# Kernel optimization log

Hardware: AMD Instinct MI355X
Metric: run time of the kernel (lower is better)

## Reference

```python
import jax, jax.numpy as jnp
import numpy as np

B, C_CLS, D_WORD, J = 1024, 80, 300, 8000
IMG_CH = 2048

def setup_inputs() -> dict:
    key = jax.random.key(0)
    ks = jax.random.split(key, 9)
    return {
        'feature': jax.random.normal(ks[0], (B, IMG_CH), jnp.float32),
        'inp': jax.random.normal(ks[1], (1, C_CLS, D_WORD), jnp.float32),
        'A': jax.random.uniform(ks[2], (C_CLS, C_CLS), jnp.float32),
        'W_gc1': jax.random.normal(ks[3], (D_WORD, 1024), jnp.float32) * (1.0 / np.sqrt(1024)),
        'W_gc2': jax.random.normal(ks[4], (1024, 2048), jnp.float32) * (1.0 / np.sqrt(2048)),
        'W_img': jax.random.normal(ks[5], (J, IMG_CH), jnp.float32) * 0.02,
        'b_img': jax.random.normal(ks[6], (J,), jnp.float32) * 0.02,
        'W_cls': jax.random.normal(ks[7], (J, 2048), jnp.float32) * 0.02,
        'b_cls': jax.random.normal(ks[8], (J,), jnp.float32) * 0.02,
    }

def _gen_adj(A):
    # torch: D = A.sum(1)**-0.5; adj = (A @ diag(D)).T @ diag(D) = D[:,None]*A.T*D[None,:]
    D = jnp.power(jnp.sum(A, axis=1), -0.5)
    return D[:, None] * A.T * D[None, :]

def reference(feature, inp, A, W_gc1, W_gc2, W_img, b_img, W_cls, b_cls):
    inp0 = inp[0]                                   # [C, 300]
    adj = jax.lax.stop_gradient(_gen_adj(A))        # [C, C], .detach() in torch
    x = adj @ (inp0 @ W_gc1)                        # gc1: [C, 1024]
    x = jax.nn.leaky_relu(x, negative_slope=0.2)
    x = adj @ (x @ W_gc2)                           # gc2: [C, 2048]
    # MFB bilinear pooling (is_usemfb=True, is_hash=False -> out_in_tmp=1, eval-mode dropout=identity)
    # original: out[b,c] = sum_j (Linear_img(feature[b])[j] * Linear_cls(x_col_c)[j])
    img_proj = feature @ W_img.T + b_img            # [B, J]
    cls_proj = x @ W_cls.T + b_cls                  # [C, J]
    x_out = img_proj @ cls_proj.T                   # [B, C]
    return x_out
```

## Files before the change

### kernel.cpp

```cpp
#include <hip/hip_runtime.h>
#include <hip/hip_bf16.h>


typedef __bf16 bf16_t;
typedef __bf16 bf16x8 __attribute__((ext_vector_type(8)));
typedef float f32x4 __attribute__((ext_vector_type(4)));

#define MFMA16(a, b, c) __builtin_amdgcn_mfma_f32_16x16x32_bf16((a), (b), (c), 0, 0, 0)

__device__ inline bf16x8 cvt8(float4 a, float4 b) {
  bf16x8 v;
  v[0] = (bf16_t)a.x; v[1] = (bf16_t)a.y; v[2] = (bf16_t)a.z; v[3] = (bf16_t)a.w;
  v[4] = (bf16_t)b.x; v[5] = (bf16_t)b.y; v[6] = (bf16_t)b.z; v[7] = (bf16_t)b.w;
  return v;
}

__global__ void k_adj(const float* __restrict__ A, float* __restrict__ adj) {
  __shared__ float Dv[80];
  int tid = threadIdx.x;
  if (tid < 80) {
    float s = 0.f;
    #pragma unroll 4
    for (int j = 0; j < 80; ++j) s += A[tid * 80 + j];
    Dv[tid] = rsqrtf(s);
  }
  __syncthreads();
  for (int idx = tid; idx < 6400; idx += blockDim.x) {
    int i = idx / 80, j = idx % 80;
    adj[idx] = Dv[i] * Dv[j] * A[j * 80 + i];
  }
}

__global__ void k_cvt0(const float* __restrict__ inp0, bf16_t* __restrict__ x0b) {
  int idx = blockIdx.x * blockDim.x + threadIdx.x;
  if (idx < 30720) {
    int c = idx / 384, k = idx % 384;
    x0b[idx] = (k < 300) ? (bf16_t)inp0[c * 300 + k] : (bf16_t)0.f;
  }
}

__global__ __launch_bounds__(256) void k_gc1m(
    const bf16_t* __restrict__ x0b, const float* __restrict__ Wgc1,
    float* __restrict__ t1) {
  int tid = threadIdx.x;
  int w = tid >> 6, l = tid & 63;
  int ln = l & 15, q = l >> 4;
  int n0 = blockIdx.x * 16;

  __shared__ float red[4][80][16];
  f32x4 acc[5] = {};
  for (int ks = 0; ks < 3; ++ks) {
    int kq = w * 96 + ks * 32 + q * 8;
    bf16x8 bfrag;
    #pragma unroll
    for (int jj = 0; jj < 8; ++jj) {
      int k = kq + jj;
      int kc = k < 300 ? k : 299;
      float wv = Wgc1[kc * 1024 + n0 + ln];
      bfrag[jj] = (bf16_t)(k < 300 ? wv : 0.f);
    }
    #pragma unroll
    for (int mt = 0; mt < 5; ++mt) {
      bf16x8 afrag = *(const bf16x8*)(x0b + (size_t)(mt * 16 + ln) * 384 + kq);
      acc[mt] = MFMA16(afrag, bfrag, acc[mt]);
    }
  }
  #pragma unroll
  for (int mt = 0; mt < 5; ++mt)
    #pragma unroll
    for (int reg = 0; reg < 4; ++reg)
      red[w][mt * 16 + q * 4 + reg][ln] = acc[mt][reg];
  __syncthreads();
  for (int o = tid; o < 1280; o += 256) {
    int c = o >> 4, nn = o & 15;
    t1[c * 1024 + n0 + nn] = red[0][c][nn] + red[1][c][nn] + red[2][c][nn] + red[3][c][nn];
  }
}

__global__ void k_adjmul_leaky(const float* __restrict__ adj, const float* __restrict__ t1,
                               bf16_t* __restrict__ x1b) {
  int idx = blockIdx.x * blockDim.x + threadIdx.x;
  int c = idx >> 10, n = idx & 1023;
  const float* ar = adj + c * 80;
  float acc = 0.f;
  #pragma unroll 4
  for (int cc = 0; cc < 80; ++cc) acc += ar[cc] * t1[cc * 1024 + n];
  x1b[idx] = (bf16_t)(acc > 0.f ? acc : 0.2f * acc);
}

__global__ __launch_bounds__(256) void k_gc2m(
    const bf16_t* __restrict__ x1b, const float* __restrict__ Wgc2,
    float* __restrict__ t2) {
  int tid = threadIdx.x;
  int w = tid >> 6, l = tid & 63;
  int ln = l & 15, q = l >> 4;
  int nc = blockIdx.x & 31, kc = blockIdx.x >> 5;

  __shared__ float Bs[32][66];
  f32x4 acc[5] = {};
  for (int s = 0; s < 2; ++s) {
    int k0 = kc * 64 + s * 32;
    #pragma unroll
    for (int it = 0; it < 2; ++it) {
      int slot = tid + it * 256;
      int kr = slot >> 4, nq = slot & 15;
      const float4 v = *(const float4*)(Wgc2 + (size_t)(k0 + kr) * 2048 + nc * 64 + nq * 4);
      *(float4*)&Bs[kr][nq * 4] = v;
    }
    __syncthreads();
    bf16x8 bfrag;
    #pragma unroll
    for (int jj = 0; jj < 8; ++jj) bfrag[jj] = (bf16_t)Bs[q * 8 + jj][w * 16 + ln];
    #pragma unroll
    for (int mt = 0; mt < 5; ++mt) {
      bf16x8 afrag = *(const bf16x8*)(x1b + (size_t)(mt * 16 + ln) * 1024 + k0 + q * 8);
      acc[mt] = MFMA16(afrag, bfrag, acc[mt]);
    }
    __syncthreads();
  }
  #pragma unroll
  for (int mt = 0; mt < 5; ++mt)
    #pragma unroll
    for (int reg = 0; reg < 4; ++reg)
      atomicAdd(&t2[(size_t)(mt * 16 + q * 4 + reg) * 2048 + nc * 64 + w * 16 + ln],
                acc[mt][reg]);
}

__global__ void k_adjmul_bf16(const float* __restrict__ adj, const float* __restrict__ t2,
                              bf16_t* __restrict__ x2) {
  int idx = blockIdx.x * blockDim.x + threadIdx.x;
  int c = idx >> 11, n = idx & 2047;
  const float* ar = adj + c * 80;
  float acc = 0.f;
  #pragma unroll 4
  for (int cc = 0; cc < 80; ++cc) acc += ar[cc] * t2[cc * 2048 + n];
  x2[idx] = (bf16_t)acc;
}

__global__ __launch_bounds__(512) void k_clsproj(
    const float* __restrict__ Wcls, const float* __restrict__ bcls,
    const float* __restrict__ bimg, const bf16_t* __restrict__ x2,
    bf16_t* __restrict__ P, float* __restrict__ r) {
  int tid = threadIdx.x;
  int w = tid >> 6, l = tid & 63;
  int ln = l & 15, q = l >> 4;
  int j0 = blockIdx.x * 16;
  size_t jrow = (size_t)(j0 + ln) * 2048;

  __shared__ float red[8][80][16];
  __shared__ float rloc[80];
  if (tid < 80) rloc[tid] = 0.f;

  f32x4 acc[5] = {};
  int kbase = w * 256 + q * 8;
  for (int ks = 0; ks < 8; ++ks) {
    int kq = kbase + ks * 32;
    const float4* bp = (const float4*)(Wcls + jrow + kq);
    float4 b0 = bp[0], b1 = bp[1];
    bf16x8 bfrag = cvt8(b0, b1);
    #pragma unroll
    for (int mt = 0; mt < 5; ++mt) {
      bf16x8 afrag = *(const bf16x8*)(x2 + (size_t)(mt * 16 + ln) * 2048 + kq);
      acc[mt] = MFMA16(afrag, bfrag, acc[mt]);
    }
  }
  #pragma unroll
  for (int mt = 0; mt < 5; ++mt)
    #pragma unroll
    for (int reg = 0; reg < 4; ++reg)
      red[w][mt * 16 + q * 4 + reg][ln] = acc[mt][reg];
  __syncthreads();

  for (int o = tid; o < 1280; o += 512) {
    int c = o >> 4, jj = o & 15;
    float v = bcls[j0 + jj];
    #pragma unroll
    for (int ww = 0; ww < 8; ++ww) v += red[ww][c][jj];
    P[(size_t)c * 8000 + j0 + jj] = (bf16_t)v;
    atomicAdd(&rloc[c], bimg[j0 + jj] * v);
  }
  __syncthreads();
  if (tid < 80) atomicAdd(&r[tid], rloc[tid]);
}

__global__ __launch_bounds__(256) void k_hmat(
    const float* __restrict__ Wimg, const bf16_t* __restrict__ P, float* __restrict__ H) {
  int tid = threadIdx.x;
  int w = tid >> 6, l = tid & 63;
  int ln = l & 15, q = l >> 4;
  int nc = blockIdx.x & 31, jc = blockIdx.x >> 5;
  int jbase = jc * 160;

  __shared__ float Bs[160][66];
  float4 v[10];
  #pragma unroll
  for (int it = 0; it < 10; ++it) {
    int slot = tid + it * 256;
    int jr = slot >> 4, nq = slot & 15;
    v[it] = *(const float4*)(Wimg + (size_t)(jbase + jr) * 2048 + nc * 64 + nq * 4);
  }
  #pragma unroll
  for (int it = 0; it < 10; ++it) {
    int slot = tid + it * 256;
    int jr = slot >> 4, nq = slot & 15;
    *(float4*)&Bs[jr][nq * 4] = v[it];
  }
  __syncthreads();

  f32x4 acc[5] = {};
  for (int s = 0; s < 5; ++s) {
    bf16x8 bfrag;
    #pragma unroll
    for (int jj = 0; jj < 8; ++jj) bfrag[jj] = (bf16_t)Bs[s * 32 + q * 8 + jj][w * 16 + ln];
    #pragma unroll
    for (int mt = 0; mt < 5; ++mt) {
      bf16x8 afrag =
          *(const bf16x8*)(P + (size_t)(mt * 16 + ln) * 8000 + jbase + s * 32 + q * 8);
      acc[mt] = MFMA16(afrag, bfrag, acc[mt]);
    }
  }
  #pragma unroll
  for (int mt = 0; mt < 5; ++mt)
    #pragma unroll
    for (int reg = 0; reg < 4; ++reg)
      atomicAdd(&H[(size_t)(mt * 16 + q * 4 + reg) * 2048 + nc * 64 + w * 16 + ln],
                acc[mt][reg]);
}

__global__ __launch_bounds__(256) void k_out(
    const float* __restrict__ feat, const float* __restrict__ H,
    const float* __restrict__ r, float* __restrict__ out) {
  int tid = threadIdx.x;
  int w = tid >> 6, l = tid & 63;
  int ln = l & 15, q = l >> 4;
  int mg = blockIdx.x & 15, kc = blockIdx.x >> 4;
  int m0 = mg * 64 + w * 16;
  size_t frow = (size_t)(m0 + ln) * 2048;

  f32x4 acc[5] = {};
  int kbase = kc * 256 + q * 8;
  for (int ks = 0; ks < 8; ++ks) {
    int kq = kbase + ks * 32;
    const float4* ap = (const float4*)(feat + frow + kq);
    bf16x8 afrag = cvt8(ap[0], ap[1]);
    #pragma unroll
    for (int nt = 0; nt < 5; ++nt) {
      const float4* hp = (const float4*)(H + (size_t)(nt * 16 + ln) * 2048 + kq);
      bf16x8 bfrag = cvt8(hp[0], hp[1]);
      acc[nt] = MFMA16(afrag, bfrag, acc[nt]);
    }
  }
  #pragma unroll
  for (int nt = 0; nt < 5; ++nt)
    #pragma unroll
    for (int reg = 0; reg < 4; ++reg) {
      int b = m0 + q * 4 + reg;
      int c = nt * 16 + ln;
      float v = acc[nt][reg];
      if (kc == 0) v += r[c];
      atomicAdd(&out[b * 80 + c], v);
    }
}

extern "C" void kernel_launch(void* const* d_in, const int* in_sizes, int n_in,
                              void* d_out, int out_size, void* d_ws, size_t ws_size,
                              hipStream_t stream) {
  const float* feature = (const float*)d_in[0];
  const float* inp     = (const float*)d_in[1];
  const float* A       = (const float*)d_in[2];
  const float* Wgc1    = (const float*)d_in[3];
  const float* Wgc2    = (const float*)d_in[4];
  const float* Wimg    = (const float*)d_in[5];
  const float* bimg    = (const float*)d_in[6];
  const float* Wcls    = (const float*)d_in[7];
  const float* bcls    = (const float*)d_in[8];
  float* out = (float*)d_out;

  char* ws = (char*)d_ws;
  float*  adj = (float*)(ws + 0);
  float*  t1  = (float*)(ws + 25600);
  bf16_t* x1b = (bf16_t*)(ws + 353280);
  float*  t2  = (float*)(ws + 517120);
  bf16_t* x2  = (bf16_t*)(ws + 1172480);
  bf16_t* P   = (bf16_t*)(ws + 1500160);
  float*  H   = (float*)(ws + 2780160);
  float*  r   = (float*)(ws + 3435520);
  bf16_t* x0b = (bf16_t*)(ws + 3435840);

  hipMemsetAsync(t2, 0, 80 * 2048 * 4, stream);
  hipMemsetAsync(H, 0, 80 * 2048 * 4, stream);
  hipMemsetAsync(r, 0, 80 * 4, stream);
  hipMemsetAsync(out, 0, 1024 * 80 * 4, stream);

  k_adj<<<1, 128, 0, stream>>>(A, adj);
  k_cvt0<<<120, 256, 0, stream>>>(inp, x0b);
  k_gc1m<<<64, 256, 0, stream>>>(x0b, Wgc1, t1);
  k_adjmul_leaky<<<320, 256, 0, stream>>>(adj, t1, x1b);
  k_gc2m<<<512, 256, 0, stream>>>(x1b, Wgc2, t2);
  k_adjmul_bf16<<<640, 256, 0, stream>>>(adj, t2, x2);
  k_clsproj<<<500, 512, 0, stream>>>(Wcls, bcls, bimg, x2, P, r);
  k_hmat<<<1600, 256, 0, stream>>>(Wimg, P, H);
  k_out<<<128, 256, 0, stream>>>(feature, H, r, out);
}
```

Measured before the change: 298.8 us.

## Replace atomic split-K accumulation with partial buffers and reduction kernels

The gc2 and H-matrix split-K kernels now write per-chunk partial sums to workspace buffers, and new reduction kernels (k_t2red, k_hred) sum them instead of using float atomicAdd. Each K chunk is doubled in size and staged through a double-buffered shared-memory tile with register prefetch of the next slice. k_out now reduces across K within a block through shared memory and writes the output directly. This removes most atomics and three memsets, at the cost of two extra launches and extra partial-buffer traffic (about 13 MB for Hp).

```diff
diff --git a/kernel.cpp b/kernel.cpp
--- a/kernel.cpp
+++ b/kernel.cpp
@@ -90,40 +90,59 @@
 
 __global__ __launch_bounds__(256) void k_gc2m(
     const bf16_t* __restrict__ x1b, const float* __restrict__ Wgc2,
-    float* __restrict__ t2) {
+    float* __restrict__ t2p) {
   int tid = threadIdx.x;
   int w = tid >> 6, l = tid & 63;
   int ln = l & 15, q = l >> 4;
   int nc = blockIdx.x & 31, kc = blockIdx.x >> 5;
-
-  __shared__ float Bs[32][66];
-  f32x4 acc[5] = {};
-  for (int s = 0; s < 2; ++s) {
-    int k0 = kc * 64 + s * 32;
+  const float* wbase = Wgc2 + (size_t)(kc * 128) * 2048 + nc * 64;
+
+  __shared__ float Bs[2][32][66];
+  float4 pv[2];
+  #pragma unroll
+  for (int it = 0; it < 2; ++it) {
+    int slot = tid + it * 256, kr = slot >> 4, nq = slot & 15;
+    pv[it] = *(const float4*)(wbase + (size_t)kr * 2048 + nq * 4);
+  }
+  f32x4 acc[5] = {};
+  for (int s = 0; s < 4; ++s) {
     #pragma unroll
     for (int it = 0; it < 2; ++it) {
-      int slot = tid + it * 256;
-      int kr = slot >> 4, nq = slot & 15;
-      const float4 v = *(const float4*)(Wgc2 + (size_t)(k0 + kr) * 2048 + nc * 64 + nq * 4);
-      *(float4*)&Bs[kr][nq * 4] = v;
+      int slot = tid + it * 256, kr = slot >> 4, nq = slot & 15;
+      *(float4*)&Bs[s & 1][kr][nq * 4] = pv[it];
     }
     __syncthreads();
+    if (s < 3) {
+      #pragma unroll
+      for (int it = 0; it < 2; ++it) {
+        int slot = tid + it * 256, kr = slot >> 4, nq = slot & 15;
+        pv[it] = *(const float4*)(wbase + (size_t)((s + 1) * 32 + kr) * 2048 + nq * 4);
+      }
+    }
+    int k0 = kc * 128 + s * 32;
     bf16x8 bfrag;
     #pragma unroll
-    for (int jj = 0; jj < 8; ++jj) bfrag[jj] = (bf16_t)Bs[q * 8 + jj][w * 16 + ln];
+    for (int jj = 0; jj < 8; ++jj) bfrag[jj] = (bf16_t)Bs[s & 1][q * 8 + jj][w * 16 + ln];
     #pragma unroll
     for (int mt = 0; mt < 5; ++mt) {
       bf16x8 afrag = *(const bf16x8*)(x1b + (size_t)(mt * 16 + ln) * 1024 + k0 + q * 8);
       acc[mt] = MFMA16(afrag, bfrag, acc[mt]);
     }
-    __syncthreads();
-  }
+  }
+  float* tp = t2p + (size_t)kc * 163840 + nc * 64 + w * 16 + ln;
   #pragma unroll
   for (int mt = 0; mt < 5; ++mt)
     #pragma unroll
     for (int reg = 0; reg < 4; ++reg)
-      atomicAdd(&t2[(size_t)(mt * 16 + q * 4 + reg) * 2048 + nc * 64 + w * 16 + ln],
-                acc[mt][reg]);
+      tp[(size_t)(mt * 16 + q * 4 + reg) * 2048] = acc[mt][reg];
+}
+
+__global__ void k_t2red(const float* __restrict__ t2p, float* __restrict__ t2) {
+  int i = blockIdx.x * 256 + threadIdx.x;
+  float s = 0.f;
+  #pragma unroll
+  for (int p = 0; p < 8; ++p) s += t2p[(size_t)p * 163840 + i];
+  t2[i] = s;
 }
 
 __global__ void k_adjmul_bf16(const float* __restrict__ adj, const float* __restrict__ t2,
@@ -184,61 +203,73 @@
 }
 
 __global__ __launch_bounds__(256) void k_hmat(
-    const float* __restrict__ Wimg, const bf16_t* __restrict__ P, float* __restrict__ H) {
+    const float* __restrict__ Wimg, const bf16_t* __restrict__ P, float* __restrict__ Hp) {
   int tid = threadIdx.x;
   int w = tid >> 6, l = tid & 63;
   int ln = l & 15, q = l >> 4;
   int nc = blockIdx.x & 31, jc = blockIdx.x >> 5;
-  int jbase = jc * 160;
-
-  __shared__ float Bs[160][66];
-  float4 v[10];
-  #pragma unroll
-  for (int it = 0; it < 10; ++it) {
-    int slot = tid + it * 256;
-    int jr = slot >> 4, nq = slot & 15;
-    v[it] = *(const float4*)(Wimg + (size_t)(jbase + jr) * 2048 + nc * 64 + nq * 4);
-  }
-  #pragma unroll
-  for (int it = 0; it < 10; ++it) {
-    int slot = tid + it * 256;
-    int jr = slot >> 4, nq = slot & 15;
-    *(float4*)&Bs[jr][nq * 4] = v[it];
-  }
-  __syncthreads();
-
-  f32x4 acc[5] = {};
-  for (int s = 0; s < 5; ++s) {
+  const float* wbase = Wimg + (size_t)(jc * 320) * 2048 + nc * 64;
+
+  __shared__ float Bs[2][32][66];
+  float4 pv[2];
+  #pragma unroll
+  for (int it = 0; it < 2; ++it) {
+    int slot = tid + it * 256, jr = slot >> 4, nq = slot & 15;
+    pv[it] = *(const float4*)(wbase + (size_t)jr * 2048 + nq * 4);
+  }
+  f32x4 acc[5] = {};
+  for (int s = 0; s < 10; ++s) {
+    #pragma unroll
+    for (int it = 0; it < 2; ++it) {
+      int slot = tid + it * 256, jr = slot >> 4, nq = slot & 15;
+      *(float4*)&Bs[s & 1][jr][nq * 4] = pv[it];
+    }
+    __syncthreads();
+    if (s < 9) {
+      #pragma unroll
+      for (int it = 0; it < 2; ++it) {
+        int slot = tid + it * 256, jr = slot >> 4, nq = slot & 15;
+        pv[it] = *(const float4*)(wbase + (size_t)((s + 1) * 32 + jr) * 2048 + nq * 4);
+      }
+    }
+    int j0 = jc * 320 + s * 32;
     bf16x8 bfrag;
     #pragma unroll
-    for (int jj = 0; jj < 8; ++jj) bfrag[jj] = (bf16_t)Bs[s * 32 + q * 8 + jj][w * 16 + ln];
+    for (int jj = 0; jj < 8; ++jj) bfrag[jj] = (bf16_t)Bs[s & 1][q * 8 + jj][w * 16 + ln];
     #pragma unroll
     for (int mt = 0; mt < 5; ++mt) {
-      bf16x8 afrag =
-          *(const bf16x8*)(P + (size_t)(mt * 16 + ln) * 8000 + jbase + s * 32 + q * 8);
+      bf16x8 afrag = *(const bf16x8*)(P + (size_t)(mt * 16 + ln) * 8000 + j0 + q * 8);
       acc[mt] = MFMA16(afrag, bfrag, acc[mt]);
     }
   }
+  float* hp = Hp + (size_t)jc * 163840 + nc * 64 + w * 16 + ln;
   #pragma unroll
   for (int mt = 0; mt < 5; ++mt)
     #pragma unroll
     for (int reg = 0; reg < 4; ++reg)
-      atomicAdd(&H[(size_t)(mt * 16 + q * 4 + reg) * 2048 + nc * 64 + w * 16 + ln],
-                acc[mt][reg]);
-}
-
-__global__ __launch_bounds__(256) void k_out(
+      hp[(size_t)(mt * 16 + q * 4 + reg) * 2048] = acc[mt][reg];
+}
+
+__global__ void k_hred(const float* __restrict__ Hp, float* __restrict__ H) {
+  int i = blockIdx.x * 256 + threadIdx.x;
+  float s = 0.f;
+  #pragma unroll
+  for (int p = 0; p < 25; ++p) s += Hp[(size_t)p * 163840 + i];
+  H[i] = s;
+}
+
+__global__ __launch_bounds__(512) void k_out(
     const float* __restrict__ feat, const float* __restrict__ H,
     const float* __restrict__ r, float* __restrict__ out) {
   int tid = threadIdx.x;
   int w = tid >> 6, l = tid & 63;
   int ln = l & 15, q = l >> 4;
-  int mg = blockIdx.x & 15, kc = blockIdx.x >> 4;
-  int m0 = mg * 64 + w * 16;
+  int m0 = blockIdx.x * 16;
   size_t frow = (size_t)(m0 + ln) * 2048;
 
-  f32x4 acc[5] = {};
-  int kbase = kc * 256 + q * 8;
+  __shared__ float red[8][16][80];
+  f32x4 acc[5] = {};
+  int kbase = w * 256 + q * 8;
   for (int ks = 0; ks < 8; ++ks) {
     int kq = kbase + ks * 32;
     const float4* ap = (const float4*)(feat + frow + kq);
@@ -253,13 +284,16 @@
   #pragma unroll
   for (int nt = 0; nt < 5; ++nt)
     #pragma unroll
-    for (int reg = 0; reg < 4; ++reg) {
-      int b = m0 + q * 4 + reg;
-      int c = nt * 16 + ln;
-      float v = acc[nt][reg];
-      if (kc == 0) v += r[c];
-      atomicAdd(&out[b * 80 + c], v);
-    }
+    for (int reg = 0; reg < 4; ++reg)
+      red[w][q * 4 + reg][nt * 16 + ln] = acc[nt][reg];
+  __syncthreads();
+  for (int o = tid; o < 1280; o += 512) {
+    int mm = o / 80, c = o % 80;
+    float v = r[c];
+    #pragma unroll
+    for (int ww = 0; ww < 8; ++ww) v += red[ww][mm][c];
+    out[(m0 + mm) * 80 + c] = v;
+  }
 }
 
 extern "C" void kernel_launch(void* const* d_in, const int* in_sizes, int n_in,
@@ -286,19 +320,20 @@
   float*  H   = (float*)(ws + 2780160);
   float*  r   = (float*)(ws + 3435520);
   bf16_t* x0b = (bf16_t*)(ws + 3435840);
-
-  hipMemsetAsync(t2, 0, 80 * 2048 * 4, stream);
-  hipMemsetAsync(H, 0, 80 * 2048 * 4, stream);
+  float*  t2p = (float*)(ws + 3497280);
+  float*  Hp  = (float*)(ws + 8740160);
+
   hipMemsetAsync(r, 0, 80 * 4, stream);
-  hipMemsetAsync(out, 0, 1024 * 80 * 4, stream);
 
   k_adj<<<1, 128, 0, stream>>>(A, adj);
   k_cvt0<<<120, 256, 0, stream>>>(inp, x0b);
   k_gc1m<<<64, 256, 0, stream>>>(x0b, Wgc1, t1);
   k_adjmul_leaky<<<320, 256, 0, stream>>>(adj, t1, x1b);
-  k_gc2m<<<512, 256, 0, stream>>>(x1b, Wgc2, t2);
+  k_gc2m<<<256, 256, 0, stream>>>(x1b, Wgc2, t2p);
+  k_t2red<<<640, 256, 0, stream>>>(t2p, t2);
   k_adjmul_bf16<<<640, 256, 0, stream>>>(adj, t2, x2);
   k_clsproj<<<500, 512, 0, stream>>>(Wcls, bcls, bimg, x2, P, r);
-  k_hmat<<<1600, 256, 0, stream>>>(Wimg, P, H);
-  k_out<<<128, 256, 0, stream>>>(feature, H, r, out);
-}
+  k_hmat<<<800, 256, 0, stream>>>(Wimg, P, Hp);
+  k_hred<<<640, 256, 0, stream>>>(Hp, H);
+  k_out<<<64, 512, 0, stream>>>(feature, H, r, out);
+}
```

Result: faster. 284.4 us (-4.8%).
